# Kernel optimization log

Hardware: AMD Instinct MI355X
Metric: run time of the kernel (lower is better)

The kernel has to match this reference:

```python
import jax, jax.numpy as jnp
import numpy as np

NEG_SLOPE = 0.05

def leaky(x):
    return jnp.where(x >= 0, x, NEG_SLOPE * x)

def segment_softmax(e, seg, num_segments):
    m = jax.ops.segment_max(e, seg, num_segments=num_segments)
    ex = jnp.exp(e - m[seg])
    s = jax.ops.segment_sum(ex, seg, num_segments=num_segments)
    return ex / s[seg]

def scatter_mean(vals, seg, num_segments):
    tot = jax.ops.segment_sum(vals, seg, num_segments=num_segments)
    cnt = jax.ops.segment_sum(jnp.ones((vals.shape[0],), vals.dtype), seg, num_segments=num_segments)
    return tot / jnp.maximum(cnt, 1.0)[:, None]

def setup_inputs() -> dict:
    key = jax.random.key(0)
    ks = jax.random.split(key, 7)
    N, E, Fn, Fe, D = 50000, 800000, 128, 64, 64
    return {
        "x": jax.random.normal(ks[0], (N, Fn), jnp.float32),
        "edge_attr": jax.random.normal(ks[1], (E, Fe), jnp.float32),
        "edge_index": jax.random.randint(ks[2], (2, E), 0, N, jnp.int64),
        "W_node": jax.random.normal(ks[3], (D, Fn), jnp.float32) * 0.05,
        "W_edge": jax.random.normal(ks[4], (D, Fe), jnp.float32) * 0.05,
        "a_node": jax.random.normal(ks[5], (2 * D,), jnp.float32) * 0.05,
        "a_edge": jax.random.normal(ks[6], (2 * D,), jnp.float32) * 0.05,
    }

def reference(x, edge_attr, edge_index, W_node, W_edge, a_node, a_edge):
    N = x.shape[0]
    E = edge_index.shape[1]
    D = W_node.shape[0]
    h = x @ W_node.T           # [N, D]
    g = edge_attr @ W_edge.T   # [E, D]

    # ----- node->node branch (with self loops) -----
    loops = jnp.arange(N, dtype=edge_index.dtype)
    i_idx = jnp.concatenate([edge_index[0], loops])  # targets [E+N]
    j_idx = jnp.concatenate([edge_index[1], loops])  # sources [E+N]
    # attention score a^T [h_i || h_j] split into halves (no concat materialized)
    hi = h @ a_node[:D]   # [N]
    hj = h @ a_node[D:]   # [N]
    e_n = leaky(hi[i_idx] + hj[j_idx])               # [E+N]
    alpha_n = segment_softmax(e_n, i_idx, N)
    x_from_nodes = scatter_mean(alpha_n[:, None] * h[j_idx], i_idx, N)  # [N, D]

    # ----- edge->node branch (each edge attends from both endpoints) -----
    i_idx_e = jnp.concatenate([edge_index[0], edge_index[1]])           # [2E]
    g2 = jnp.concatenate([g, g], axis=0)                                # g[k_idx_e], [2E, D]
    he = h @ a_edge[:D]   # [N]
    ge = g @ a_edge[D:]   # [E]
    ge2 = jnp.concatenate([ge, ge])
    e_e = leaky(he[i_idx_e] + ge2)                                      # [2E]
    alpha_e = segment_softmax(e_e, i_idx_e, N)
    x_from_edges = scatter_mean(alpha_e[:, None] * g2, i_idx_e, N)      # [N, D]

    return jnp.concatenate([leaky(x_from_nodes), leaky(x_from_edges)], axis=-1)  # [N, 2D]
```

## Files before the change

### kernel.cpp

```cpp
#include <hip/hip_runtime.h>
#include <math.h>

#define NEG_SLOPE 0.05f

__device__ __forceinline__ float leaky(float x){ return x >= 0.f ? x : NEG_SLOPE * x; }

__device__ __forceinline__ unsigned short f2bf(float f){
    unsigned u = __float_as_uint(f);
    unsigned r = u + 0x7FFFu + ((u >> 16) & 1u);
    return (unsigned short)(r >> 16);
}
__device__ __forceinline__ float bf2f(unsigned short us){
    return __uint_as_float((unsigned)us << 16);
}

__global__ __launch_bounds__(256) void k_init(int* deg_n, int* deg_o, int* ctr,
        float* __restrict__ vv, const float* __restrict__ We, const float* __restrict__ a_edge, int N){
    int t = blockIdx.x * blockDim.x + threadIdx.x;
    if (t == 0){ ctr[0] = 0; ctr[1] = 0; }
    if (t < 64){
        float s = 0.f;
        for (int d = 0; d < 64; d++) s = fmaf(We[d * 64 + t], a_edge[64 + d], s);
        vv[t] = s;
    }
    int stride = gridDim.x * blockDim.x;
    for (int i = t; i < N; i += stride){ deg_n[i] = 0; deg_o[i] = 0; }
}

__global__ __launch_bounds__(256) void k_gemm_h(const float* __restrict__ A, const float* __restrict__ B,
        const float* __restrict__ a_node, const float* __restrict__ a_edge,
        float* __restrict__ C, unsigned short* __restrict__ Cb,
        float* __restrict__ hi, float* __restrict__ hj, float* __restrict__ he, int M){
    const int K = 128;
    __shared__ float As[K][68];
    __shared__ float Bs[K][68];
    const int m0 = blockIdx.x * 64;
    const int t = threadIdx.x;
    for (int i = t; i < 16 * K; i += 256){
        int d = i & 63, kq = i >> 6;
        float4 b = *(const float4*)&B[(size_t)d * K + kq * 4];
        Bs[kq*4+0][d] = b.x; Bs[kq*4+1][d] = b.y; Bs[kq*4+2][d] = b.z; Bs[kq*4+3][d] = b.w;
    }
    for (int i = t; i < 16 * K; i += 256){
        int r = i & 63, kq = i >> 6;
        int m = m0 + r;
        float4 a = make_float4(0.f, 0.f, 0.f, 0.f);
        if (m < M) a = *(const float4*)&A[(size_t)m * K + kq * 4];
        As[kq*4+0][r] = a.x; As[kq*4+1][r] = a.y; As[kq*4+2][r] = a.z; As[kq*4+3][r] = a.w;
    }
    __syncthreads();
    const int tx = t & 15, ty = t >> 4;
    float acc[4][4] = {};
    #pragma unroll 4
    for (int k = 0; k < K; k++){
        float4 a4 = *(const float4*)&As[k][ty * 4];
        float4 b4 = *(const float4*)&Bs[k][tx * 4];
        float av[4] = {a4.x, a4.y, a4.z, a4.w};
        float bv[4] = {b4.x, b4.y, b4.z, b4.w};
        #pragma unroll
        for (int r = 0; r < 4; r++)
            #pragma unroll
            for (int c = 0; c < 4; c++)
                acc[r][c] = fmaf(av[r], bv[c], acc[r][c]);
    }
    #pragma unroll
    for (int r = 0; r < 4; r++){
        int m = m0 + ty * 4 + r;
        if (m < M){
            float4 o = make_float4(acc[r][0], acc[r][1], acc[r][2], acc[r][3]);
            *(float4*)&C[(size_t)m * 64 + tx * 4] = o;
            uint2 u;
            u.x = (unsigned)f2bf(o.x) | ((unsigned)f2bf(o.y) << 16);
            u.y = (unsigned)f2bf(o.z) | ((unsigned)f2bf(o.w) << 16);
            *(uint2*)&Cb[(size_t)m * 64 + tx * 4] = u;
        }
    }
    float4 an1 = *(const float4*)&a_node[tx * 4];
    float4 an2 = *(const float4*)&a_node[64 + tx * 4];
    float4 ae1 = *(const float4*)&a_edge[tx * 4];
    float p1[4], p2[4], p3[4];
    #pragma unroll
    for (int r = 0; r < 4; r++){
        p1[r] = acc[r][0]*an1.x + acc[r][1]*an1.y + acc[r][2]*an1.z + acc[r][3]*an1.w;
        p2[r] = acc[r][0]*an2.x + acc[r][1]*an2.y + acc[r][2]*an2.z + acc[r][3]*an2.w;
        p3[r] = acc[r][0]*ae1.x + acc[r][1]*ae1.y + acc[r][2]*ae1.z + acc[r][3]*ae1.w;
    }
    #pragma unroll
    for (int m = 1; m < 16; m <<= 1){
        #pragma unroll
        for (int r = 0; r < 4; r++){
            p1[r] += __shfl_xor(p1[r], m);
            p2[r] += __shfl_xor(p2[r], m);
            p3[r] += __shfl_xor(p3[r], m);
        }
    }
    if (tx == 0){
        #pragma unroll
        for (int r = 0; r < 4; r++){
            int m = m0 + ty * 4 + r;
            if (m < M){ hi[m] = p1[r]; hj[m] = p2[r]; he[m] = p3[r]; }
        }
    }
}

__global__ __launch_bounds__(256) void k_ge2(const float* __restrict__ ea, const int* __restrict__ idx,
        const float* __restrict__ vv, float* __restrict__ ge, unsigned short* __restrict__ eab,
        int* __restrict__ deg_n, int* __restrict__ deg_o, int E){
    int l = threadIdx.x & 63;
    int gw = (blockIdx.x * 256 + threadIdx.x) >> 6;
    int nw = (gridDim.x * 256) >> 6;
    int seg = l & 15, rl = l >> 4;
    float4 v4 = *(const float4*)&vv[seg * 4];
    for (int r0 = gw * 4; r0 < E; r0 += nw * 4){
        int row = r0 + rl;
        if (row < E){
            float4 a = *(const float4*)&ea[(size_t)row * 64 + seg * 4];
            float s = a.x*v4.x + a.y*v4.y + a.z*v4.z + a.w*v4.w;
            uint2 u;
            u.x = (unsigned)f2bf(a.x) | ((unsigned)f2bf(a.y) << 16);
            u.y = (unsigned)f2bf(a.z) | ((unsigned)f2bf(a.w) << 16);
            *(uint2*)&eab[(size_t)row * 64 + seg * 4] = u;
            #pragma unroll
            for (int m = 1; m < 16; m <<= 1) s += __shfl_xor(s, m);
            if (seg == 0){
                ge[row] = s;
                int i0 = idx[row], i1 = idx[E + row];
                atomicAdd(&deg_n[i0], 1);
                atomicAdd(&deg_o[i1], 1);
            }
        }
    }
}

__global__ __launch_bounds__(256) void k_off(const int* __restrict__ deg_n, const int* __restrict__ deg_o,
        int* __restrict__ deg_e,
        int* __restrict__ off_n, int* __restrict__ cur_n,
        int* __restrict__ off_e, int* __restrict__ cur_e,
        int* __restrict__ ctr, int N){
    int i = blockIdx.x * 256 + threadIdx.x;
    int lane = threadIdx.x & 63;
    int dn = 0, de = 0;
    if (i < N){
        dn = deg_n[i];
        de = dn + deg_o[i];
    }
    int pn = dn, pe = de;
    #pragma unroll
    for (int d = 1; d < 64; d <<= 1){
        int on = __shfl_up(pn, d), oe = __shfl_up(pe, d);
        if (lane >= d){ pn += on; pe += oe; }
    }
    int base_n = 0, base_e = 0;
    if (lane == 63){
        base_n = atomicAdd(&ctr[0], pn);
        base_e = atomicAdd(&ctr[1], pe);
    }
    base_n = __shfl(base_n, 63);
    base_e = __shfl(base_e, 63);
    if (i < N){
        int on = base_n + pn - dn;
        int oe = base_e + pe - de;
        off_n[i] = on; cur_n[i] = on;
        off_e[i] = oe; cur_e[i] = oe;
        deg_e[i] = de;
    }
}

__global__ __launch_bounds__(256) void k_fill(const int* __restrict__ idx,
        const float* __restrict__ hj, const float* __restrict__ ge,
        int* __restrict__ cur_n, int* __restrict__ cur_e,
        int2* __restrict__ adj_n, int2* __restrict__ adj_e, int E, int N){
    int g = blockIdx.x & 7;
    int lo = (int)(((long long)g * N) >> 3), hi = (int)(((long long)(g + 1) * N) >> 3);
    int nblk = gridDim.x >> 3;
    int start = ((blockIdx.x >> 3) * 256) + threadIdx.x;
    int stride = nblk * 256;
    for (int k = start; k < E; k += stride){
        int i0 = idx[k], i1 = idx[E + k];
        bool t0 = (i0 >= lo && i0 < hi), t1 = (i1 >= lo && i1 < hi);
        if (t0 | t1){
            int gb = __float_as_int(ge[k]);
            if (t0){
                adj_n[atomicAdd(&cur_n[i0], 1)] = make_int2(i1, __float_as_int(hj[i1]));
                adj_e[atomicAdd(&cur_e[i0], 1)] = make_int2(k, gb);
            }
            if (t1) adj_e[atomicAdd(&cur_e[i1], 1)] = make_int2(k, gb);
        }
    }
}

__global__ __launch_bounds__(256) void k_out(const float* __restrict__ h,
        const unsigned short* __restrict__ hb, const unsigned short* __restrict__ eab,
        const float* __restrict__ hi, const float* __restrict__ hj, const float* __restrict__ he,
        const float* __restrict__ We,
        const int* __restrict__ off_n, const int* __restrict__ deg_n, const int2* __restrict__ adj_n,
        const int* __restrict__ off_e, const int* __restrict__ deg_e, const int2* __restrict__ adj_e,
        float* __restrict__ out, int N, int nb_node){
    __shared__ float WeT[64][65];
    __shared__ float valS[4][64];
    int lane = threadIdx.x & 63;
    int w = threadIdx.x >> 6;

    if (blockIdx.x < nb_node){
        int i = (blockIdx.x * 256 + (int)threadIdx.x) >> 6;
        if (i >= N) return;
        float hi_i = hi[i];
        float wself = __expf(leaky(hi_i + hj[i]));
        float s = wself;
        float acc = wself * h[(size_t)i * 64 + lane];
        int cnt = deg_n[i];
        int p = off_n[i], e = p + cnt;
        for (; p + 4 <= e; p += 4){
            int2 r0 = adj_n[p], r1 = adj_n[p+1], r2 = adj_n[p+2], r3 = adj_n[p+3];
            float v0 = bf2f(hb[(size_t)r0.x * 64 + lane]);
            float v1 = bf2f(hb[(size_t)r1.x * 64 + lane]);
            float v2 = bf2f(hb[(size_t)r2.x * 64 + lane]);
            float v3 = bf2f(hb[(size_t)r3.x * 64 + lane]);
            float w0 = __expf(leaky(hi_i + __int_as_float(r0.y)));
            float w1 = __expf(leaky(hi_i + __int_as_float(r1.y)));
            float w2 = __expf(leaky(hi_i + __int_as_float(r2.y)));
            float w3 = __expf(leaky(hi_i + __int_as_float(r3.y)));
            acc = fmaf(w0, v0, acc); acc = fmaf(w1, v1, acc);
            acc = fmaf(w2, v2, acc); acc = fmaf(w3, v3, acc);
            s += (w0 + w1) + (w2 + w3);
        }
        for (; p < e; p++){
            int2 r = adj_n[p];
            float v = bf2f(hb[(size_t)r.x * 64 + lane]);
            float wgt = __expf(leaky(hi_i + __int_as_float(r.y)));
            acc = fmaf(wgt, v, acc); s += wgt;
        }
        out[(size_t)i * 128 + lane] = leaky(acc / s / (float)(cnt + 1));
    } else {
        for (int t2 = threadIdx.x; t2 < 1024; t2 += 256){
            int d = t2 >> 4, c0 = (t2 & 15) * 4;
            float4 v = *(const float4*)&We[d * 64 + c0];
            WeT[c0+0][d] = v.x; WeT[c0+1][d] = v.y; WeT[c0+2][d] = v.z; WeT[c0+3][d] = v.w;
        }
        int i = ((blockIdx.x - nb_node) * 256 + (int)threadIdx.x) >> 6;
        float val = 0.f;
        int iok = (i < N);
        if (iok){
            float he_i = he[i];
            float s = 0.f, acc = 0.f;
            int cnt = deg_e[i];
            int p = off_e[i], e = p + cnt;
            for (; p + 4 <= e; p += 4){
                int2 r0 = adj_e[p], r1 = adj_e[p+1], r2 = adj_e[p+2], r3 = adj_e[p+3];
                float v0 = bf2f(eab[(size_t)r0.x * 64 + lane]);
                float v1 = bf2f(eab[(size_t)r1.x * 64 + lane]);
                float v2 = bf2f(eab[(size_t)r2.x * 64 + lane]);
                float v3 = bf2f(eab[(size_t)r3.x * 64 + lane]);
                float w0 = __expf(leaky(he_i + __int_as_float(r0.y)));
                float w1 = __expf(leaky(he_i + __int_as_float(r1.y)));
                float w2 = __expf(leaky(he_i + __int_as_float(r2.y)));
                float w3 = __expf(leaky(he_i + __int_as_float(r3.y)));
                acc = fmaf(w0, v0, acc); acc = fmaf(w1, v1, acc);
                acc = fmaf(w2, v2, acc); acc = fmaf(w3, v3, acc);
                s += (w0 + w1) + (w2 + w3);
            }
            for (; p < e; p++){
                int2 r = adj_e[p];
                float v = bf2f(eab[(size_t)r.x * 64 + lane]);
                float wgt = __expf(leaky(he_i + __int_as_float(r.y)));
                acc = fmaf(wgt, v, acc); s += wgt;
            }
            val = (cnt > 0) ? (acc / s / (float)cnt) : 0.f;
        }
        __syncthreads();
        valS[w][lane] = val;
        __syncthreads();
        if (iok){
            float acc2 = 0.f;
            #pragma unroll
            for (int c4 = 0; c4 < 16; c4++){
                float4 vb = *(const float4*)&valS[w][c4 * 4];
                acc2 = fmaf(vb.x, WeT[c4*4+0][lane], acc2);
                acc2 = fmaf(vb.y, WeT[c4*4+1][lane], acc2);
                acc2 = fmaf(vb.z, WeT[c4*4+2][lane], acc2);
                acc2 = fmaf(vb.w, WeT[c4*4+3][lane], acc2);
            }
            out[(size_t)i * 128 + 64 + lane] = leaky(acc2);
        }
    }
}

extern "C" void kernel_launch(void* const* d_in, const int* in_sizes, int n_in,
                              void* d_out, int out_size, void* d_ws, size_t ws_size,
                              hipStream_t stream){
    const float* x      = (const float*)d_in[0];
    const float* ea     = (const float*)d_in[1];
    const int*   idx    = (const int*)  d_in[2];
    const float* Wn     = (const float*)d_in[3];
    const float* We     = (const float*)d_in[4];
    const float* a_node = (const float*)d_in[5];
    const float* a_edge = (const float*)d_in[6];
    float* out = (float*)d_out;

    const int N = in_sizes[0] / 128;
    const int E = in_sizes[1] / 64;

    float* p = (float*)d_ws;
    float* h      = p; p += (size_t)N * 64;
    float* hi     = p; p += N;
    float* hj     = p; p += N;
    float* he     = p; p += N;
    float* ge     = p; p += E;
    float* vv     = p; p += 64;
    unsigned short* hb  = (unsigned short*)p; p += (size_t)N * 32;
    unsigned short* eab = (unsigned short*)p; p += (size_t)E * 32;
    int* deg_n = (int*)p; p += N;
    int* deg_o = (int*)p; p += N;
    int* deg_e = (int*)p; p += N;
    int* off_n = (int*)p; p += N;
    int* off_e = (int*)p; p += N;
    int* cur_n = (int*)p; p += N;
    int* cur_e = (int*)p; p += N;
    int* ctr   = (int*)p; p += 4;
    int2* adj_n = (int2*)p; p += (size_t)2 * E;
    int2* adj_e = (int2*)p; p += (size_t)4 * E;

    const int nb = (N + 3) / 4;

    k_init<<<256, 256, 0, stream>>>(deg_n, deg_o, ctr, vv, We, a_edge, N);
    k_gemm_h<<<(N + 63) / 64, 256, 0, stream>>>(x, Wn, a_node, a_edge, h, hb, hi, hj, he, N);
    k_ge2<<<2048, 256, 0, stream>>>(ea, idx, vv, ge, eab, deg_n, deg_o, E);
    k_off<<<(N + 255) / 256, 256, 0, stream>>>(deg_n, deg_o, deg_e, off_n, cur_n, off_e, cur_e, ctr, N);
    k_fill<<<1024, 256, 0, stream>>>(idx, hj, ge, cur_n, cur_e, adj_n, adj_e, E, N);
    k_out<<<2 * nb, 256, 0, stream>>>(h, hb, eab, hi, hj, he, We,
                                      off_n, deg_n, adj_n, off_e, deg_e, adj_e, out, N, nb);
}
```

Before: 611.8 us.

## Gather four neighbors per wave with vector bf16 loads and drop init kernel

The aggregation kernel now assigns each quarter-wave to a different neighbor, with each lane loading four bf16 features via 8-byte loads. Partial sums are combined with cross-quarter shuffles. This is meant to raise memory-level parallelism in the latency-bound neighbor gather. Separately, the init kernel is removed: degree zeroing moves into the GEMM kernel and the edge projection vector is recomputed per block in shared memory. That saves one launch at the cost of redundant small work per block.

```diff
diff --git a/kernel.cpp b/kernel.cpp
--- a/kernel.cpp
+++ b/kernel.cpp
@@ -14,28 +14,19 @@
     return __uint_as_float((unsigned)us << 16);
 }
 
-__global__ __launch_bounds__(256) void k_init(int* deg_n, int* deg_o, int* ctr,
-        float* __restrict__ vv, const float* __restrict__ We, const float* __restrict__ a_edge, int N){
-    int t = blockIdx.x * blockDim.x + threadIdx.x;
-    if (t == 0){ ctr[0] = 0; ctr[1] = 0; }
-    if (t < 64){
-        float s = 0.f;
-        for (int d = 0; d < 64; d++) s = fmaf(We[d * 64 + t], a_edge[64 + d], s);
-        vv[t] = s;
-    }
-    int stride = gridDim.x * blockDim.x;
-    for (int i = t; i < N; i += stride){ deg_n[i] = 0; deg_o[i] = 0; }
-}
-
 __global__ __launch_bounds__(256) void k_gemm_h(const float* __restrict__ A, const float* __restrict__ B,
         const float* __restrict__ a_node, const float* __restrict__ a_edge,
         float* __restrict__ C, unsigned short* __restrict__ Cb,
-        float* __restrict__ hi, float* __restrict__ hj, float* __restrict__ he, int M){
+        float* __restrict__ hi, float* __restrict__ hj, float* __restrict__ he,
+        int* __restrict__ deg_n, int* __restrict__ deg_o, int* __restrict__ ctr, int M){
     const int K = 128;
     __shared__ float As[K][68];
     __shared__ float Bs[K][68];
     const int m0 = blockIdx.x * 64;
     const int t = threadIdx.x;
+    int gt = blockIdx.x * 256 + t;
+    if (gt < M){ deg_n[gt] = 0; deg_o[gt] = 0; }
+    if (gt == 0){ ctr[0] = 0; ctr[1] = 0; }
     for (int i = t; i < 16 * K; i += 256){
         int d = i & 63, kq = i >> 6;
         float4 b = *(const float4*)&B[(size_t)d * K + kq * 4];
@@ -104,13 +95,22 @@
 }
 
 __global__ __launch_bounds__(256) void k_ge2(const float* __restrict__ ea, const int* __restrict__ idx,
-        const float* __restrict__ vv, float* __restrict__ ge, unsigned short* __restrict__ eab,
+        const float* __restrict__ We, const float* __restrict__ a_edge,
+        float* __restrict__ ge, unsigned short* __restrict__ eab,
         int* __restrict__ deg_n, int* __restrict__ deg_o, int E){
-    int l = threadIdx.x & 63;
-    int gw = (blockIdx.x * 256 + threadIdx.x) >> 6;
+    __shared__ float vvs[64];
+    int t = threadIdx.x;
+    if (t < 64){
+        float s = 0.f;
+        for (int d = 0; d < 64; d++) s = fmaf(We[d * 64 + t], a_edge[64 + d], s);
+        vvs[t] = s;
+    }
+    __syncthreads();
+    int l = t & 63;
+    int gw = (blockIdx.x * 256 + t) >> 6;
     int nw = (gridDim.x * 256) >> 6;
     int seg = l & 15, rl = l >> 4;
-    float4 v4 = *(const float4*)&vv[seg * 4];
+    float4 v4 = *(const float4*)&vvs[seg * 4];
     for (int r0 = gw * 4; r0 < E; r0 += nw * 4){
         int row = r0 + rl;
         if (row < E){
@@ -198,39 +198,106 @@
         float* __restrict__ out, int N, int nb_node){
     __shared__ float WeT[64][65];
     __shared__ float valS[4][64];
-    int lane = threadIdx.x & 63;
-    int w = threadIdx.x >> 6;
+    const int lane = threadIdx.x & 63;
+    const int w = threadIdx.x >> 6;
+    const int rl = lane >> 4, seg = lane & 15;
 
     if (blockIdx.x < nb_node){
         int i = (blockIdx.x * 256 + (int)threadIdx.x) >> 6;
         if (i >= N) return;
         float hi_i = hi[i];
-        float wself = __expf(leaky(hi_i + hj[i]));
-        float s = wself;
-        float acc = wself * h[(size_t)i * 64 + lane];
         int cnt = deg_n[i];
-        int p = off_n[i], e = p + cnt;
-        for (; p + 4 <= e; p += 4){
-            int2 r0 = adj_n[p], r1 = adj_n[p+1], r2 = adj_n[p+2], r3 = adj_n[p+3];
-            float v0 = bf2f(hb[(size_t)r0.x * 64 + lane]);
-            float v1 = bf2f(hb[(size_t)r1.x * 64 + lane]);
-            float v2 = bf2f(hb[(size_t)r2.x * 64 + lane]);
-            float v3 = bf2f(hb[(size_t)r3.x * 64 + lane]);
-            float w0 = __expf(leaky(hi_i + __int_as_float(r0.y)));
-            float w1 = __expf(leaky(hi_i + __int_as_float(r1.y)));
-            float w2 = __expf(leaky(hi_i + __int_as_float(r2.y)));
-            float w3 = __expf(leaky(hi_i + __int_as_float(r3.y)));
-            acc = fmaf(w0, v0, acc); acc = fmaf(w1, v1, acc);
-            acc = fmaf(w2, v2, acc); acc = fmaf(w3, v3, acc);
-            s += (w0 + w1) + (w2 + w3);
-        }
-        for (; p < e; p++){
-            int2 r = adj_n[p];
-            float v = bf2f(hb[(size_t)r.x * 64 + lane]);
-            float wgt = __expf(leaky(hi_i + __int_as_float(r.y)));
-            acc = fmaf(wgt, v, acc); s += wgt;
-        }
-        out[(size_t)i * 128 + lane] = leaky(acc / s / (float)(cnt + 1));
+        int p = off_n[i];
+        int e = p + cnt;
+        float a0 = 0.f, a1 = 0.f, a2 = 0.f, a3 = 0.f, sp = 0.f;
+        for (; p + 16 <= e; p += 16){
+            int2 q0 = adj_n[p + rl];
+            int2 q1 = adj_n[p + 4 + rl];
+            int2 q2 = adj_n[p + 8 + rl];
+            int2 q3 = adj_n[p + 12 + rl];
+            uint2 u0 = *(const uint2*)&hb[(size_t)q0.x * 64 + seg * 4];
+            uint2 u1 = *(const uint2*)&hb[(size_t)q1.x * 64 + seg * 4];
+            uint2 u2 = *(const uint2*)&hb[(size_t)q2.x * 64 + seg * 4];
+            uint2 u3 = *(const uint2*)&hb[(size_t)q3.x * 64 + seg * 4];
+            float w0 = __expf(leaky(hi_i + __int_as_float(q0.y)));
+            float w1 = __expf(leaky(hi_i + __int_as_float(q1.y)));
+            float w2 = __expf(leaky(hi_i + __int_as_float(q2.y)));
+            float w3 = __expf(leaky(hi_i + __int_as_float(q3.y)));
+            a0 = fmaf(w0, bf2f((unsigned short)u0.x), a0);
+            a1 = fmaf(w0, bf2f((unsigned short)(u0.x >> 16)), a1);
+            a2 = fmaf(w0, bf2f((unsigned short)u0.y), a2);
+            a3 = fmaf(w0, bf2f((unsigned short)(u0.y >> 16)), a3);
+            a0 = fmaf(w1, bf2f((unsigned short)u1.x), a0);
+            a1 = fmaf(w1, bf2f((unsigned short)(u1.x >> 16)), a1);
+            a2 = fmaf(w1, bf2f((unsigned short)u1.y), a2);
+            a3 = fmaf(w1, bf2f((unsigned short)(u1.y >> 16)), a3);
+            a0 = fmaf(w2, bf2f((unsigned short)u2.x), a0);
+            a1 = fmaf(w2, bf2f((unsigned short)(u2.x >> 16)), a1);
+            a2 = fmaf(w2, bf2f((unsigned short)u2.y), a2);
+            a3 = fmaf(w2, bf2f((unsigned short)(u2.y >> 16)), a3);
+            a0 = fmaf(w3, bf2f((unsigned short)u3.x), a0);
+            a1 = fmaf(w3, bf2f((unsigned short)(u3.x >> 16)), a1);
+            a2 = fmaf(w3, bf2f((unsigned short)u3.y), a2);
+            a3 = fmaf(w3, bf2f((unsigned short)(u3.y >> 16)), a3);
+            sp += (w0 + w1) + (w2 + w3);
+        }
+        if (p + 8 <= e){
+            int2 q0 = adj_n[p + rl];
+            int2 q1 = adj_n[p + 4 + rl];
+            uint2 u0 = *(const uint2*)&hb[(size_t)q0.x * 64 + seg * 4];
+            uint2 u1 = *(const uint2*)&hb[(size_t)q1.x * 64 + seg * 4];
+            float w0 = __expf(leaky(hi_i + __int_as_float(q0.y)));
+            float w1 = __expf(leaky(hi_i + __int_as_float(q1.y)));
+            a0 = fmaf(w0, bf2f((unsigned short)u0.x), a0);
+            a1 = fmaf(w0, bf2f((unsigned short)(u0.x >> 16)), a1);
+            a2 = fmaf(w0, bf2f((unsigned short)u0.y), a2);
+            a3 = fmaf(w0, bf2f((unsigned short)(u0.y >> 16)), a3);
+            a0 = fmaf(w1, bf2f((unsigned short)u1.x), a0);
+            a1 = fmaf(w1, bf2f((unsigned short)(u1.x >> 16)), a1);
+            a2 = fmaf(w1, bf2f((unsigned short)u1.y), a2);
+            a3 = fmaf(w1, bf2f((unsigned short)(u1.y >> 16)), a3);
+            sp += w0 + w1;
+            p += 8;
+        }
+        if (p + 4 <= e){
+            int2 q0 = adj_n[p + rl];
+            uint2 u0 = *(const uint2*)&hb[(size_t)q0.x * 64 + seg * 4];
+            float w0 = __expf(leaky(hi_i + __int_as_float(q0.y)));
+            a0 = fmaf(w0, bf2f((unsigned short)u0.x), a0);
+            a1 = fmaf(w0, bf2f((unsigned short)(u0.x >> 16)), a1);
+            a2 = fmaf(w0, bf2f((unsigned short)u0.y), a2);
+            a3 = fmaf(w0, bf2f((unsigned short)(u0.y >> 16)), a3);
+            sp += w0;
+            p += 4;
+        }
+        int rem = e - p;
+        if (rl < rem){
+            int2 q0 = adj_n[p + rl];
+            uint2 u0 = *(const uint2*)&hb[(size_t)q0.x * 64 + seg * 4];
+            float w0 = __expf(leaky(hi_i + __int_as_float(q0.y)));
+            a0 = fmaf(w0, bf2f((unsigned short)u0.x), a0);
+            a1 = fmaf(w0, bf2f((unsigned short)(u0.x >> 16)), a1);
+            a2 = fmaf(w0, bf2f((unsigned short)u0.y), a2);
+            a3 = fmaf(w0, bf2f((unsigned short)(u0.y >> 16)), a3);
+            sp += w0;
+        }
+        a0 += __shfl_xor(a0, 16); a0 += __shfl_xor(a0, 32);
+        a1 += __shfl_xor(a1, 16); a1 += __shfl_xor(a1, 32);
+        a2 += __shfl_xor(a2, 16); a2 += __shfl_xor(a2, 32);
+        a3 += __shfl_xor(a3, 16); a3 += __shfl_xor(a3, 32);
+        sp += __shfl_xor(sp, 16); sp += __shfl_xor(sp, 32);
+        if (rl == 0){
+            float4 h4 = *(const float4*)&h[(size_t)i * 64 + seg * 4];
+            float wself = __expf(leaky(hi_i + hj[i]));
+            float s = sp + wself;
+            float inv = 1.f / (s * (float)(cnt + 1));
+            float4 o;
+            o.x = leaky(fmaf(wself, h4.x, a0) * inv);
+            o.y = leaky(fmaf(wself, h4.y, a1) * inv);
+            o.z = leaky(fmaf(wself, h4.z, a2) * inv);
+            o.w = leaky(fmaf(wself, h4.w, a3) * inv);
+            *(float4*)&out[(size_t)i * 128 + seg * 4] = o;
+        }
     } else {
         for (int t2 = threadIdx.x; t2 < 1024; t2 += 256){
             int d = t2 >> 4, c0 = (t2 & 15) * 4;
@@ -238,37 +305,97 @@
             WeT[c0+0][d] = v.x; WeT[c0+1][d] = v.y; WeT[c0+2][d] = v.z; WeT[c0+3][d] = v.w;
         }
         int i = ((blockIdx.x - nb_node) * 256 + (int)threadIdx.x) >> 6;
-        float val = 0.f;
-        int iok = (i < N);
+        const int iok = (i < N);
+        float v0 = 0.f, v1 = 0.f, v2 = 0.f, v3 = 0.f;
         if (iok){
             float he_i = he[i];
-            float s = 0.f, acc = 0.f;
             int cnt = deg_e[i];
-            int p = off_e[i], e = p + cnt;
-            for (; p + 4 <= e; p += 4){
-                int2 r0 = adj_e[p], r1 = adj_e[p+1], r2 = adj_e[p+2], r3 = adj_e[p+3];
-                float v0 = bf2f(eab[(size_t)r0.x * 64 + lane]);
-                float v1 = bf2f(eab[(size_t)r1.x * 64 + lane]);
-                float v2 = bf2f(eab[(size_t)r2.x * 64 + lane]);
-                float v3 = bf2f(eab[(size_t)r3.x * 64 + lane]);
-                float w0 = __expf(leaky(he_i + __int_as_float(r0.y)));
-                float w1 = __expf(leaky(he_i + __int_as_float(r1.y)));
-                float w2 = __expf(leaky(he_i + __int_as_float(r2.y)));
-                float w3 = __expf(leaky(he_i + __int_as_float(r3.y)));
-                acc = fmaf(w0, v0, acc); acc = fmaf(w1, v1, acc);
-                acc = fmaf(w2, v2, acc); acc = fmaf(w3, v3, acc);
-                s += (w0 + w1) + (w2 + w3);
-            }
-            for (; p < e; p++){
-                int2 r = adj_e[p];
-                float v = bf2f(eab[(size_t)r.x * 64 + lane]);
-                float wgt = __expf(leaky(he_i + __int_as_float(r.y)));
-                acc = fmaf(wgt, v, acc); s += wgt;
-            }
-            val = (cnt > 0) ? (acc / s / (float)cnt) : 0.f;
+            int p = off_e[i];
+            int e = p + cnt;
+            float a0 = 0.f, a1 = 0.f, a2 = 0.f, a3 = 0.f, sp = 0.f;
+            for (; p + 16 <= e; p += 16){
+                int2 q0 = adj_e[p + rl];
+                int2 q1 = adj_e[p + 4 + rl];
+                int2 q2 = adj_e[p + 8 + rl];
+                int2 q3 = adj_e[p + 12 + rl];
+                uint2 u0 = *(const uint2*)&eab[(size_t)q0.x * 64 + seg * 4];
+                uint2 u1 = *(const uint2*)&eab[(size_t)q1.x * 64 + seg * 4];
+                uint2 u2 = *(const uint2*)&eab[(size_t)q2.x * 64 + seg * 4];
+                uint2 u3 = *(const uint2*)&eab[(size_t)q3.x * 64 + seg * 4];
+                float w0 = __expf(leaky(he_i + __int_as_float(q0.y)));
+                float w1 = __expf(leaky(he_i + __int_as_float(q1.y)));
+                float w2 = __expf(leaky(he_i + __int_as_float(q2.y)));
+                float w3 = __expf(leaky(he_i + __int_as_float(q3.y)));
+                a0 = fmaf(w0, bf2f((unsigned short)u0.x), a0);
+                a1 = fmaf(w0, bf2f((unsigned short)(u0.x >> 16)), a1);
+                a2 = fmaf(w0, bf2f((unsigned short)u0.y), a2);
+                a3 = fmaf(w0, bf2f((unsigned short)(u0.y >> 16)), a3);
+                a0 = fmaf(w1, bf2f((unsigned short)u1.x), a0);
+                a1 = fmaf(w1, bf2f((unsigned short)(u1.x >> 16)), a1);
+                a2 = fmaf(w1, bf2f((unsigned short)u1.y), a2);
+                a3 = fmaf(w1, bf2f((unsigned short)(u1.y >> 16)), a3);
+                a0 = fmaf(w2, bf2f((unsigned short)u2.x), a0);
+                a1 = fmaf(w2, bf2f((unsigned short)(u2.x >> 16)), a1);
+                a2 = fmaf(w2, bf2f((unsigned short)u2.y), a2);
+                a3 = fmaf(w2, bf2f((unsigned short)(u2.y >> 16)), a3);
+                a0 = fmaf(w3, bf2f((unsigned short)u3.x), a0);
+                a1 = fmaf(w3, bf2f((unsigned short)(u3.x >> 16)), a1);
+                a2 = fmaf(w3, bf2f((unsigned short)u3.y), a2);
+                a3 = fmaf(w3, bf2f((unsigned short)(u3.y >> 16)), a3);
+                sp += (w0 + w1) + (w2 + w3);
+            }
+            if (p + 8 <= e){
+                int2 q0 = adj_e[p + rl];
+                int2 q1 = adj_e[p + 4 + rl];
+                uint2 u0 = *(const uint2*)&eab[(size_t)q0.x * 64 + seg * 4];
+                uint2 u1 = *(const uint2*)&eab[(size_t)q1.x * 64 + seg * 4];
+                float w0 = __expf(leaky(he_i + __int_as_float(q0.y)));
+                float w1 = __expf(leaky(he_i + __int_as_float(q1.y)));
+                a0 = fmaf(w0, bf2f((unsigned short)u0.x), a0);
+                a1 = fmaf(w0, bf2f((unsigned short)(u0.x >> 16)), a1);
+                a2 = fmaf(w0, bf2f((unsigned short)u0.y), a2);
+                a3 = fmaf(w0, bf2f((unsigned short)(u0.y >> 16)), a3);
+                a0 = fmaf(w1, bf2f((unsigned short)u1.x), a0);
+                a1 = fmaf(w1, bf2f((unsigned short)(u1.x >> 16)), a1);
+                a2 = fmaf(w1, bf2f((unsigned short)u1.y), a2);
+                a3 = fmaf(w1, bf2f((unsigned short)(u1.y >> 16)), a3);
+                sp += w0 + w1;
+                p += 8;
+            }
+            if (p + 4 <= e){
+                int2 q0 = adj_e[p + rl];
+                uint2 u0 = *(const uint2*)&eab[(size_t)q0.x * 64 + seg * 4];
+                float w0 = __expf(leaky(he_i + __int_as_float(q0.y)));
+                a0 = fmaf(w0, bf2f((unsigned short)u0.x), a0);
+                a1 = fmaf(w0, bf2f((unsigned short)(u0.x >> 16)), a1);
+                a2 = fmaf(w0, bf2f((unsigned short)u0.y), a2);
+                a3 = fmaf(w0, bf2f((unsigned short)(u0.y >> 16)), a3);
+                sp += w0;
+                p += 4;
+            }
+            int rem = e - p;
+            if (rl < rem){
+                int2 q0 = adj_e[p + rl];
+                uint2 u0 = *(const uint2*)&eab[(size_t)q0.x * 64 + seg * 4];
+                float w0 = __expf(leaky(he_i + __int_as_float(q0.y)));
+                a0 = fmaf(w0, bf2f((unsigned short)u0.x), a0);
+                a1 = fmaf(w0, bf2f((unsigned short)(u0.x >> 16)), a1);
+                a2 = fmaf(w0, bf2f((unsigned short)u0.y), a2);
+                a3 = fmaf(w0, bf2f((unsigned short)(u0.y >> 16)), a3);
+                sp += w0;
+            }
+            a0 += __shfl_xor(a0, 16); a0 += __shfl_xor(a0, 32);
+            a1 += __shfl_xor(a1, 16); a1 += __shfl_xor(a1, 32);
+            a2 += __shfl_xor(a2, 16); a2 += __shfl_xor(a2, 32);
+            a3 += __shfl_xor(a3, 16); a3 += __shfl_xor(a3, 32);
+            sp += __shfl_xor(sp, 16); sp += __shfl_xor(sp, 32);
+            if (cnt > 0){
+                float inv = 1.f / (sp * (float)cnt);
+                v0 = a0 * inv; v1 = a1 * inv; v2 = a2 * inv; v3 = a3 * inv;
+            }
         }
         __syncthreads();
-        valS[w][lane] = val;
+        if (rl == 0) *(float4*)&valS[w][seg * 4] = make_float4(v0, v1, v2, v3);
         __syncthreads();
         if (iok){
             float acc2 = 0.f;
@@ -306,7 +433,6 @@
     float* hj     = p; p += N;
     float* he     = p; p += N;
     float* ge     = p; p += E;
-    float* vv     = p; p += 64;
     unsigned short* hb  = (unsigned short*)p; p += (size_t)N * 32;
     unsigned short* eab = (unsigned short*)p; p += (size_t)E * 32;
     int* deg_n = (int*)p; p += N;
@@ -322,9 +448,9 @@
 
     const int nb = (N + 3) / 4;
 
-    k_init<<<256, 256, 0, stream>>>(deg_n, deg_o, ctr, vv, We, a_edge, N);
-    k_gemm_h<<<(N + 63) / 64, 256, 0, stream>>>(x, Wn, a_node, a_edge, h, hb, hi, hj, he, N);
-    k_ge2<<<2048, 256, 0, stream>>>(ea, idx, vv, ge, eab, deg_n, deg_o, E);
+    k_gemm_h<<<(N + 63) / 64, 256, 0, stream>>>(x, Wn, a_node, a_edge, h, hb, hi, hj, he,
+                                                deg_n, deg_o, ctr, N);
+    k_ge2<<<2048, 256, 0, stream>>>(ea, idx, We, a_edge, ge, eab, deg_n, deg_o, E);
     k_off<<<(N + 255) / 256, 256, 0, stream>>>(deg_n, deg_o, deg_e, off_n, cur_n, off_e, cur_e, ctr, N);
     k_fill<<<1024, 256, 0, stream>>>(idx, hj, ge, cur_n, cur_e, adj_n, adj_e, E, N);
     k_out<<<2 * nb, 256, 0, stream>>>(h, hb, eab, hi, hj, he, We,
```

Measured after the change: 578.1 us. 1.06x faster.
